# Performance work log

Measured on AMD Instinct MI355X. Metric: run time of the kernel, lower is better.

## Reference

```python
import jax, jax.numpy as jnp
import numpy as np

B, L, C = 4, 2048, 512
H, D = 8, 512          # n_head, hidden_dim (per-head dim)
TEMP = 1.0
EPS = 1e-5


def setup_inputs() -> dict:
    key = jax.random.key(0)
    ks = jax.random.split(key, 12)
    s_in = 1.0 / np.sqrt(C)
    s_out = 1.0 / np.sqrt(H * D)
    return {
        "q": jax.random.normal(ks[0], (B, L, C), jnp.float32),
        "k": jax.random.normal(ks[1], (B, L, C), jnp.float32),
        "v": jax.random.normal(ks[2], (B, L, C), jnp.float32),
        "mask": jax.random.randint(ks[3], (B, L, L), 0, 2).astype(bool),
        "Wq": jax.random.normal(ks[4], (C, H * D), jnp.float32) * s_in,
        "bq": jnp.zeros((H * D,), jnp.float32),
        "Wk": jax.random.normal(ks[5], (C, H * D), jnp.float32) * s_in,
        "bk": jnp.zeros((H * D,), jnp.float32),
        "Wv": jax.random.normal(ks[6], (C, H * D), jnp.float32) * s_in,
        "bv": jnp.zeros((H * D,), jnp.float32),
        "Wo": jax.random.normal(ks[7], (H * D, D), jnp.float32) * s_out,
        "bo": jnp.zeros((D,), jnp.float32),
        "gamma": jnp.ones((D,), jnp.float32),
        "beta": jnp.zeros((D,), jnp.float32),
    }


def reference(q, k, v, mask, Wq, bq, Wk, bk, Wv, bv, Wo, bo, gamma, beta):
    b, ql, _ = q.shape
    residual = q
    qh = (q @ Wq + bq).reshape(b, ql, H, D)           # b,l,h,d
    kh = (k @ Wk + bk).reshape(b, ql, H, D)
    vh = (v @ Wv + bv).reshape(b, ql, H, D)
    # scores in head-major layout to mirror torch permute(2,0,1,3)
    scores = jnp.einsum("bqhd,bkhd->hbqk", qh, kh) / TEMP  # h,b,l,l
    scores = jnp.where(mask[None], -jnp.inf, scores)
    atten = jax.nn.softmax(scores, axis=-1)                 # h,b,l,l
    ctx = jnp.einsum("hbqk,bkhd->bqhd", atten, vh)          # b,l,h,d
    ctx = ctx.reshape(b, ql, H * D)
    out = ctx @ Wo + bo                                     # b,l,D  (dropout in eval mode)
    x = out + residual
    mu = jnp.mean(x, axis=-1, keepdims=True)
    var = jnp.var(x, axis=-1, keepdims=True)
    out = (x - mu) / jnp.sqrt(var + EPS) * gamma + beta
    return out, atten.reshape(H * b, ql, ql)
```

## Files before the change

### kernel.cpp

```cpp
#include <hip/hip_runtime.h>
#include <stdint.h>


typedef unsigned short u16;
typedef _Float16 f16;
typedef __attribute__((ext_vector_type(4))) _Float16 f16x4;
typedef __attribute__((ext_vector_type(8))) _Float16 f16x8;
typedef __attribute__((ext_vector_type(4))) float f32x4;

#define EPI_QKH    0
#define EPI_VHT    1
#define EPI_SCORES 2
#define EPI_CTX    3
#define EPI_OUT    4

__device__ __forceinline__ f32x4 mfma16(f16x8 a, f16x8 b, f32x4 c) {
  return __builtin_amdgcn_mfma_f32_16x16x32_f16(a, b, c, 0, 0, 0);
}

__device__ __forceinline__ void stage_tile_f16(const char* gbase, size_t grow, char* lds, int tid) {
  const int lane = tid & 63, wave = tid >> 6;
#pragma unroll
  for (int c = 0; c < 2; ++c) {
    int chunk = wave * 2 + c;
    int off = chunk * 1024 + lane * 16;
    int r = off >> 6;
    int cb = off & 63;
    const char* g = gbase + (size_t)r * grow + cb;
    __builtin_amdgcn_global_load_lds(
        (__attribute__((address_space(1))) void*)g,
        (__attribute__((address_space(3))) void*)(lds + chunk * 1024),
        16, 0, 0);
  }
}

__device__ __forceinline__ f16x8 load_frag16(const char* lds, int row, int kq) {
  return *(const f16x8*)(lds + ((size_t)row * 32 + kq) * 2);
}

template<int EPI>
__global__ __launch_bounds__(512, 2)
void gemm256_k(const char* __restrict__ A, const char* __restrict__ B,
               int lda, int ldb, int K,
               char* __restrict__ C0, const float* __restrict__ bias) {
  __shared__ alignas(16) char smem[3][32768];

  const int tid = threadIdx.x, lane = tid & 63, wave = tid >> 6;
  const int wm = wave >> 2, wn = wave & 3;

  const int nx = gridDim.x, ny = gridDim.y;
  int id = blockIdx.x + nx * blockIdx.y;
  const int chunk = (nx * ny) >> 3;
  id = (id & 7) * chunk + (id >> 3);
  const int m0 = (id % nx) * 256, n0 = (id / nx) * 256;

  const char* pA = A; const char* pB = B;
  if constexpr (EPI == EPI_SCORES) {
    int z = blockIdx.z, h = z >> 2, b = z & 3;
    size_t e2 = ((size_t)b * 2048 * 4096 + (size_t)h * 512) * 2;
    pA += e2; pB += e2;
  } else if constexpr (EPI == EPI_CTX) {
    int z = blockIdx.z, h = z >> 2, b = z & 3;
    pA += ((size_t)z << 22) * 2;
    pB += ((size_t)(b * 8 + h) * 512 * 2048) * 2;
  }

  f32x4 acc[8][4];
#pragma unroll
  for (int i = 0; i < 8; ++i)
#pragma unroll
    for (int j = 0; j < 4; ++j) acc[i][j] = (f32x4){0.f, 0.f, 0.f, 0.f};

  const size_t rowA = (size_t)lda * 2, rowB = (size_t)ldb * 2;
  const char* gA = pA + (size_t)m0 * rowA;
  const char* gB = pB + (size_t)n0 * rowB;

  const int nk = K >> 5;
  const int kq = (lane >> 4) * 8, l15 = lane & 15, quad = lane >> 4;

  stage_tile_f16(gA, rowA, smem[0], tid);
  stage_tile_f16(gB, rowB, smem[0] + 16384, tid);
  stage_tile_f16(gA + 64, rowA, smem[1], tid);
  stage_tile_f16(gB + 64, rowB, smem[1] + 16384, tid);

  int bc = 0;
  for (int kt = 0; kt < nk; ++kt) {
    if (kt + 1 < nk) { asm volatile("s_waitcnt vmcnt(4)" ::: "memory"); }
    else             { asm volatile("s_waitcnt vmcnt(0)" ::: "memory"); }
    __builtin_amdgcn_sched_barrier(0);
    __builtin_amdgcn_s_barrier();
    __builtin_amdgcn_sched_barrier(0);

    if (kt + 2 < nk) {
      int b2 = bc + 2; if (b2 >= 3) b2 -= 3;
      char* nb = smem[b2];
      stage_tile_f16(gA + (size_t)(kt + 2) * 64, rowA, nb, tid);
      stage_tile_f16(gB + (size_t)(kt + 2) * 64, rowB, nb + 16384, tid);
    }

    char* cur = smem[bc];
    f16x8 af[8], bf[4];
#pragma unroll
    for (int mi = 0; mi < 8; ++mi)
      af[mi] = load_frag16(cur, wm * 128 + mi * 16 + l15, kq);
#pragma unroll
    for (int ni = 0; ni < 4; ++ni)
      bf[ni] = load_frag16(cur + 16384, wn * 64 + ni * 16 + l15, kq);

    __builtin_amdgcn_s_setprio(1);
#pragma unroll
    for (int mi = 0; mi < 8; ++mi)
#pragma unroll
      for (int ni = 0; ni < 4; ++ni)
        acc[mi][ni] = mfma16(af[mi], bf[ni], acc[mi][ni]);
    __builtin_amdgcn_s_setprio(0);

    bc = (bc + 1 == 3) ? 0 : bc + 1;
  }

#pragma unroll
  for (int mi = 0; mi < 8; ++mi)
#pragma unroll
    for (int ni = 0; ni < 4; ++ni)
#pragma unroll
      for (int r = 0; r < 4; ++r) {
        int m = m0 + wm * 128 + mi * 16 + quad * 4 + r;
        int n = n0 + wn * 64 + ni * 16 + l15;
        float v = acc[mi][ni][r];
        if constexpr (EPI == EPI_QKH) {
          v += bias[n];
          ((f16*)C0)[(size_t)m * 4096 + n] = (f16)v;
        } else if constexpr (EPI == EPI_VHT) {
          v += bias[m];
          int hh = m >> 9, d = m & 511, bb = n >> 11, ll = n & 2047;
          ((f16*)C0)[(((size_t)(bb * 8 + hh) * 512 + d) << 11) + ll] = (f16)v;
        } else if constexpr (EPI == EPI_SCORES) {
          int z = blockIdx.z;
          ((float*)C0)[((size_t)z << 22) + ((size_t)m << 11) + n] = v;
        } else if constexpr (EPI == EPI_CTX) {
          int z = blockIdx.z, hh = z >> 2, bb = z & 3;
          ((f16*)C0)[((size_t)(bb * 2048 + m) << 12) + hh * 512 + n] = (f16)v;
        }
      }
}

template<int EPI>
__global__ __launch_bounds__(256, 2)
void gemm_k(const char* __restrict__ A, const char* __restrict__ B,
            int lda, int ldb, int K,
            char* __restrict__ C0,
            const float* __restrict__ bias, const float* __restrict__ resid) {
  __shared__ alignas(16) char smem[3 * 16384];

  const int tid = threadIdx.x, lane = tid & 63, wave = tid >> 6;
  const int wm = wave >> 1, wn = wave & 1;

  const int nx = gridDim.x, ny = gridDim.y;
  int id = blockIdx.x + nx * blockIdx.y;
  const int chunk = (nx * ny) >> 3;
  id = (id & 7) * chunk + (id >> 3);
  const int m0 = (id % nx) * 128, n0 = (id / nx) * 128;

  const char* pA = A; const char* pB = B;
  int kz = 0;
  if constexpr (EPI == EPI_OUT) {
    kz = blockIdx.z;
    pA += (size_t)kz * 2048 * 2;
    pB += (size_t)kz * 2048 * 2;
  }

  f32x4 acc[4][4];
#pragma unroll
  for (int i = 0; i < 4; ++i)
#pragma unroll
    for (int j = 0; j < 4; ++j) acc[i][j] = (f32x4){0.f, 0.f, 0.f, 0.f};

  const size_t rowA = (size_t)lda * 2, rowB = (size_t)ldb * 2;
  const char* gA = pA + (size_t)m0 * rowA;
  const char* gB = pB + (size_t)n0 * rowB;

  const int nk = K >> 5;
  const int kq = (lane >> 4) * 8, l15 = lane & 15, quad = lane >> 4;

  stage_tile_f16(gA, rowA, smem, tid);
  stage_tile_f16(gB, rowB, smem + 8192, tid);
  stage_tile_f16(gA + 64, rowA, smem + 16384, tid);
  stage_tile_f16(gB + 64, rowB, smem + 16384 + 8192, tid);

  int bc = 0;
  for (int kt = 0; kt < nk; ++kt) {
    if (kt + 1 < nk) { asm volatile("s_waitcnt vmcnt(4)" ::: "memory"); }
    else             { asm volatile("s_waitcnt vmcnt(0)" ::: "memory"); }
    __builtin_amdgcn_sched_barrier(0);
    __builtin_amdgcn_s_barrier();
    __builtin_amdgcn_sched_barrier(0);

    if (kt + 2 < nk) {
      int b2 = bc + 2; if (b2 >= 3) b2 -= 3;
      char* nb = smem + b2 * 16384;
      stage_tile_f16(gA + (size_t)(kt + 2) * 64, rowA, nb, tid);
      stage_tile_f16(gB + (size_t)(kt + 2) * 64, rowB, nb + 8192, tid);
    }

    char* cur = smem + bc * 16384;
    f16x8 af[4], bf[4];
#pragma unroll
    for (int mi = 0; mi < 4; ++mi)
      af[mi] = load_frag16(cur, wm * 64 + mi * 16 + l15, kq);
#pragma unroll
    for (int ni = 0; ni < 4; ++ni)
      bf[ni] = load_frag16(cur + 8192, wn * 64 + ni * 16 + l15, kq);

    __builtin_amdgcn_s_setprio(1);
#pragma unroll
    for (int mi = 0; mi < 4; ++mi)
#pragma unroll
      for (int ni = 0; ni < 4; ++ni)
        acc[mi][ni] = mfma16(af[mi], bf[ni], acc[mi][ni]);
    __builtin_amdgcn_s_setprio(0);

    bc = (bc + 1 == 3) ? 0 : bc + 1;
  }

#pragma unroll
  for (int mi = 0; mi < 4; ++mi)
#pragma unroll
    for (int ni = 0; ni < 4; ++ni)
#pragma unroll
      for (int r = 0; r < 4; ++r) {
        int m = m0 + wm * 64 + mi * 16 + quad * 4 + r;
        int n = n0 + wn * 64 + ni * 16 + l15;
        float v = acc[mi][ni][r];
        if constexpr (EPI == EPI_OUT) {
          if (kz == 0) v += bias[n] + resid[((size_t)m << 9) + n];
          ((float*)C0)[(size_t)kz * 8192 * 512 + ((size_t)m << 9) + n] = v;
        }
      }
}

__global__ __launch_bounds__(256)
void transpose_cvt_k(const float* __restrict__ in, f16* __restrict__ T,
                     int R, int Cc) {
  __shared__ f16 tile[32][33];
  const int t = threadIdx.x, tc = t & 31, tr = t >> 5;
  const int bx = blockIdx.x, by = blockIdx.y;
#pragma unroll
  for (int k = 0; k < 4; ++k) {
    int r = by * 32 + tr + k * 8;
    tile[tr + k * 8][tc] = (f16)in[(size_t)r * Cc + bx * 32 + tc];
  }
  __syncthreads();
#pragma unroll
  for (int k = 0; k < 4; ++k) {
    int c = bx * 32 + tr + k * 8;
    T[(size_t)c * R + by * 32 + tc] = tile[tc][tr + k * 8];
  }
}

__global__ __launch_bounds__(256)
void cvt_f16_k(const float* __restrict__ in, f16* __restrict__ out) {
  int i = blockIdx.x * 256 + threadIdx.x;
  float4 v = ((const float4*)in)[i];
  f16x4 h;
  h[0] = (f16)v.x; h[1] = (f16)v.y; h[2] = (f16)v.z; h[3] = (f16)v.w;
  ((f16x4*)out)[i] = h;
}

__global__ __launch_bounds__(256)
void maskprep_k(const int* __restrict__ m32, unsigned char* __restrict__ m8) {
  int i = blockIdx.x * 256 + threadIdx.x;
  int4 v = ((const int4*)m32)[i];
  uchar4 c;
  c.x = (unsigned char)v.x; c.y = (unsigned char)v.y;
  c.z = (unsigned char)v.z; c.w = (unsigned char)v.w;
  ((uchar4*)m8)[i] = c;
}

__global__ __launch_bounds__(256)
void softmax_k(float* __restrict__ att, const unsigned char* __restrict__ m8,
               f16* __restrict__ att16) {
  __shared__ float sm[4];
  int t = threadIdx.x, lane = t & 63, wave = t >> 6;
  size_t r = blockIdx.x;
  int z = (int)(r >> 11), m = (int)(r & 2047), b = z & 3;
  float4* row = (float4*)(att + (r << 11));
  const uchar4* mrow = (const uchar4*)(m8 + (((size_t)b << 22) + ((size_t)m << 11)));
  float4 a = row[t], c = row[t + 256];
  uchar4 ma = mrow[t], mc = mrow[t + 256];
  if (ma.x) a.x = -1e30f; if (ma.y) a.y = -1e30f;
  if (ma.z) a.z = -1e30f; if (ma.w) a.w = -1e30f;
  if (mc.x) c.x = -1e30f; if (mc.y) c.y = -1e30f;
  if (mc.z) c.z = -1e30f; if (mc.w) c.w = -1e30f;
  float mx = fmaxf(fmaxf(fmaxf(a.x, a.y), fmaxf(a.z, a.w)),
                   fmaxf(fmaxf(c.x, c.y), fmaxf(c.z, c.w)));
#pragma unroll
  for (int o = 32; o > 0; o >>= 1) mx = fmaxf(mx, __shfl_xor(mx, o));
  if (lane == 0) sm[wave] = mx;
  __syncthreads();
  mx = fmaxf(fmaxf(sm[0], sm[1]), fmaxf(sm[2], sm[3]));
  a.x = __expf(a.x - mx); a.y = __expf(a.y - mx);
  a.z = __expf(a.z - mx); a.w = __expf(a.w - mx);
  c.x = __expf(c.x - mx); c.y = __expf(c.y - mx);
  c.z = __expf(c.z - mx); c.w = __expf(c.w - mx);
  float s = a.x + a.y + a.z + a.w + c.x + c.y + c.z + c.w;
#pragma unroll
  for (int o = 32; o > 0; o >>= 1) s += __shfl_xor(s, o);
  __syncthreads();
  if (lane == 0) sm[wave] = s;
  __syncthreads();
  s = sm[0] + sm[1] + sm[2] + sm[3];
  float inv = 1.0f / s;
  a.x *= inv; a.y *= inv; a.z *= inv; a.w *= inv;
  c.x *= inv; c.y *= inv; c.z *= inv; c.w *= inv;
  row[t] = a; row[t + 256] = c;
  f16x4* r16 = (f16x4*)(att16 + (r << 11));
  f16x4 ha, hc;
  ha[0] = (f16)a.x; ha[1] = (f16)a.y; ha[2] = (f16)a.z; ha[3] = (f16)a.w;
  hc[0] = (f16)c.x; hc[1] = (f16)c.y; hc[2] = (f16)c.z; hc[3] = (f16)c.w;
  r16[t] = ha; r16[t + 256] = hc;
}

__global__ __launch_bounds__(256)
void ln_k(const float* __restrict__ x0, const float* __restrict__ x1,
          const float* __restrict__ gamma, const float* __restrict__ beta,
          float* __restrict__ out) {
  __shared__ float s1[4], s2[4];
  int t = threadIdx.x, lane = t & 63, wave = t >> 6;
  size_t base = (size_t)blockIdx.x << 9;
  float2 va = ((const float2*)(x0 + base))[t];
  float2 vb = ((const float2*)(x1 + base))[t];
  float2 v; v.x = va.x + vb.x; v.y = va.y + vb.y;
  float s = v.x + v.y;
  float q = v.x * v.x + v.y * v.y;
#pragma unroll
  for (int o = 32; o > 0; o >>= 1) { s += __shfl_xor(s, o); q += __shfl_xor(q, o); }
  if (lane == 0) { s1[wave] = s; s2[wave] = q; }
  __syncthreads();
  s = s1[0] + s1[1] + s1[2] + s1[3];
  q = s2[0] + s2[1] + s2[2] + s2[3];
  float mu = s * (1.0f / 512.0f);
  float var = q * (1.0f / 512.0f) - mu * mu;
  float rs = rsqrtf(var + 1e-5f);
  float2 g = ((const float2*)gamma)[t];
  float2 bb = ((const float2*)beta)[t];
  float2 o2;
  o2.x = (v.x - mu) * rs * g.x + bb.x;
  o2.y = (v.y - mu) * rs * g.y + bb.y;
  ((float2*)(out + base))[t] = o2;
}

extern "C" void kernel_launch(void* const* d_in, const int* in_sizes, int n_in,
                              void* d_out, int out_size, void* d_ws, size_t ws_size,
                              hipStream_t stream) {
  (void)in_sizes; (void)n_in; (void)out_size; (void)ws_size;
  const float* q     = (const float*)d_in[0];
  const float* k     = (const float*)d_in[1];
  const float* v     = (const float*)d_in[2];
  const int*   mask  = (const int*)d_in[3];
  const float* Wq    = (const float*)d_in[4];
  const float* bq    = (const float*)d_in[5];
  const float* Wk    = (const float*)d_in[6];
  const float* bk    = (const float*)d_in[7];
  const float* Wv    = (const float*)d_in[8];
  const float* bv    = (const float*)d_in[9];
  const float* Wo    = (const float*)d_in[10];
  const float* bo    = (const float*)d_in[11];
  const float* gamma = (const float*)d_in[12];
  const float* beta  = (const float*)d_in[13];

  float* out0  = (float*)d_out;
  float* atten = out0 + (size_t)4 * 2048 * 512;

  char* ws = (char*)d_ws;
  const size_t MB = 1024ull * 1024ull;
  f16* WqT  = (f16*)(ws + 0 * MB);
  f16* WkT  = (f16*)(ws + 4 * MB);
  f16* WvT  = (f16*)(ws + 8 * MB);
  f16* WoT  = (f16*)(ws + 12 * MB);
  unsigned char* mask8 = (unsigned char*)(ws + 16 * MB);
  f16* q16  = (f16*)(ws + 32 * MB);
  f16* k16  = (f16*)(ws + 40 * MB);
  f16* v16  = (f16*)(ws + 48 * MB);
  f16* vhT  = (f16*)(ws + 56 * MB);
  f16* atten16 = (f16*)(ws + 120 * MB);
  f16* qh   = (f16*)(ws + 120 * MB);
  f16* kh   = (f16*)(ws + 184 * MB);
  f16* ctx  = (f16*)(ws + 376 * MB);
  float* xbuf = (float*)(ws + 120 * MB);

  transpose_cvt_k<<<dim3(128, 16), 256, 0, stream>>>(Wq, WqT, 512, 4096);
  transpose_cvt_k<<<dim3(128, 16), 256, 0, stream>>>(Wk, WkT, 512, 4096);
  transpose_cvt_k<<<dim3(128, 16), 256, 0, stream>>>(Wv, WvT, 512, 4096);
  transpose_cvt_k<<<dim3(16, 128), 256, 0, stream>>>(Wo, WoT, 4096, 512);
  maskprep_k<<<16384, 256, 0, stream>>>(mask, mask8);
  cvt_f16_k<<<4096, 256, 0, stream>>>(q, q16);
  cvt_f16_k<<<4096, 256, 0, stream>>>(k, k16);
  cvt_f16_k<<<4096, 256, 0, stream>>>(v, v16);

  gemm256_k<EPI_QKH><<<dim3(32, 16, 1), 512, 0, stream>>>(
      (const char*)q16, (const char*)WqT, 512, 512, 512, (char*)qh, bq);
  gemm256_k<EPI_QKH><<<dim3(32, 16, 1), 512, 0, stream>>>(
      (const char*)k16, (const char*)WkT, 512, 512, 512, (char*)kh, bk);

  gemm256_k<EPI_VHT><<<dim3(16, 32, 1), 512, 0, stream>>>(
      (const char*)WvT, (const char*)v16, 512, 512, 512, (char*)vhT, bv);

  gemm256_k<EPI_SCORES><<<dim3(8, 8, 32), 512, 0, stream>>>(
      (const char*)qh, (const char*)kh, 4096, 4096, 512, (char*)atten, nullptr);

  softmax_k<<<65536, 256, 0, stream>>>(atten, mask8, atten16);

  gemm256_k<EPI_CTX><<<dim3(8, 2, 32), 512, 0, stream>>>(
      (const char*)atten16, (const char*)vhT, 2048, 2048, 2048, (char*)ctx, nullptr);

  gemm_k<EPI_OUT><<<dim3(64, 4, 2), 256, 0, stream>>>(
      (const char*)ctx, (const char*)WoT, 4096, 4096, 2048, (char*)xbuf, bo, q);

  ln_k<<<8192, 256, 0, stream>>>(xbuf, xbuf + (size_t)8192 * 512, gamma, beta, out0);
}
```

Before: 1.495 ms.

## Restructure 256-tile GEMM into K=64 double-buffered, XOR-swizzled, four-phase pipeline

Replaces the triple-buffered K=32 tile loop of the 256x256 GEMM with a double-buffered K=64 scheme. Each tile is split into four 128-row halves that are staged one at a time between four MFMA phases, so loads for the next tile overlap compute on the current one. LDS rows are 128 bytes with an XOR swizzle on the column to reduce bank conflicts on fragment reads. The cost is more barriers per iteration and 128KB of LDS per block, which may limit occupancy relative to the previous 96KB.

Result: no change. 1.486 ms (-0.6%).

```diff
diff --git a/kernel.cpp b/kernel.cpp
--- a/kernel.cpp
+++ b/kernel.cpp
@@ -18,40 +18,41 @@
   return __builtin_amdgcn_mfma_f32_16x16x32_f16(a, b, c, 0, 0, 0);
 }
 
-__device__ __forceinline__ void stage_tile_f16(const char* gbase, size_t grow, char* lds, int tid) {
-  const int lane = tid & 63, wave = tid >> 6;
+__device__ __forceinline__ void stage_half(const char* ghalf, size_t grow,
+                                           char* ldshalf, int tid) {
 #pragma unroll
   for (int c = 0; c < 2; ++c) {
-    int chunk = wave * 2 + c;
-    int off = chunk * 1024 + lane * 16;
-    int r = off >> 6;
-    int cb = off & 63;
-    const char* g = gbase + (size_t)r * grow + cb;
+    int d = c * 8192 + tid * 16;
+    int r = d >> 7;
+    int c2l = (d & 127) ^ ((r & 7) << 4);
+    const char* g = ghalf + (size_t)r * grow + c2l;
     __builtin_amdgcn_global_load_lds(
         (__attribute__((address_space(1))) void*)g,
-        (__attribute__((address_space(3))) void*)(lds + chunk * 1024),
+        (__attribute__((address_space(3))) void*)(ldshalf + d),
         16, 0, 0);
   }
 }
 
-__device__ __forceinline__ f16x8 load_frag16(const char* lds, int row, int kq) {
-  return *(const f16x8*)(lds + ((size_t)row * 32 + kq) * 2);
+__device__ __forceinline__ f16x8 frag_swz(const char* ldshalf, int r, int kbyte) {
+  return *(const f16x8*)(ldshalf + r * 128 + (kbyte ^ ((r & 7) << 4)));
 }
 
 template<int EPI>
 __global__ __launch_bounds__(512, 2)
-void gemm256_k(const char* __restrict__ A, const char* __restrict__ B,
-               int lda, int ldb, int K,
-               char* __restrict__ C0, const float* __restrict__ bias) {
-  __shared__ alignas(16) char smem[3][32768];
+void gemm256p_k(const char* __restrict__ A, const char* __restrict__ B,
+                int lda, int ldb, int K,
+                char* __restrict__ C0, const float* __restrict__ bias) {
+  __shared__ alignas(16) char smem[2][65536];
 
   const int tid = threadIdx.x, lane = tid & 63, wave = tid >> 6;
   const int wm = wave >> 2, wn = wave & 3;
+  const int l15 = lane & 15, quad = lane >> 4;
+  const int kb = quad * 16;
 
   const int nx = gridDim.x, ny = gridDim.y;
   int id = blockIdx.x + nx * blockIdx.y;
-  const int chunk = (nx * ny) >> 3;
-  id = (id & 7) * chunk + (id >> 3);
+  const int chunkw = (nx * ny) >> 3;
+  id = (id & 7) * chunkw + (id >> 3);
   const int m0 = (id % nx) * 256, n0 = (id / nx) * 256;
 
   const char* pA = A; const char* pB = B;
@@ -72,50 +73,115 @@
     for (int j = 0; j < 4; ++j) acc[i][j] = (f32x4){0.f, 0.f, 0.f, 0.f};
 
   const size_t rowA = (size_t)lda * 2, rowB = (size_t)ldb * 2;
-  const char* gA = pA + (size_t)m0 * rowA;
-  const char* gB = pB + (size_t)n0 * rowB;
-
-  const int nk = K >> 5;
-  const int kq = (lane >> 4) * 8, l15 = lane & 15, quad = lane >> 4;
-
-  stage_tile_f16(gA, rowA, smem[0], tid);
-  stage_tile_f16(gB, rowB, smem[0] + 16384, tid);
-  stage_tile_f16(gA + 64, rowA, smem[1], tid);
-  stage_tile_f16(gB + 64, rowB, smem[1] + 16384, tid);
-
-  int bc = 0;
-  for (int kt = 0; kt < nk; ++kt) {
-    if (kt + 1 < nk) { asm volatile("s_waitcnt vmcnt(4)" ::: "memory"); }
-    else             { asm volatile("s_waitcnt vmcnt(0)" ::: "memory"); }
+  const char* gA0 = pA + (size_t)m0 * rowA;
+  const char* gA1 = gA0 + (size_t)128 * rowA;
+  const char* gB0 = pB + (size_t)n0 * rowB;
+  const char* gB1 = gB0 + (size_t)128 * rowB;
+
+  const int nt = K >> 6;
+
+  stage_half(gA0, rowA, smem[0],         tid);
+  stage_half(gA1, rowA, smem[0] + 16384, tid);
+  stage_half(gB0, rowB, smem[0] + 32768, tid);
+  stage_half(gB1, rowB, smem[0] + 49152, tid);
+  if (nt > 1) {
+    stage_half(gA0 + 128, rowA, smem[1], tid);
+    asm volatile("s_waitcnt vmcnt(2)" ::: "memory");
+  } else {
+    asm volatile("s_waitcnt vmcnt(0)" ::: "memory");
+  }
+  __builtin_amdgcn_sched_barrier(0);
+  __builtin_amdgcn_s_barrier();
+  __builtin_amdgcn_sched_barrier(0);
+
+  for (int t = 0; t < nt; ++t) {
+    char* cb = smem[t & 1];
+    char* nb = smem[(t + 1) & 1];
+    const char* myA = cb + wm * 16384;
+    const char* myB = cb + 32768 + (wn >> 1) * 16384;
+    const int rb = (wn & 1) * 64;
+    const size_t ko1 = (size_t)(t + 1) * 128;
+    const size_t ko2 = (size_t)(t + 2) * 128;
+
+    f16x8 a[8], b01[4], b23[4];
+
+    if (t + 1 < nt) stage_half(gA1 + ko1, rowA, nb + 16384, tid);
+#pragma unroll
+    for (int mi = 0; mi < 4; ++mi) {
+      a[mi * 2]     = frag_swz(myA, mi * 16 + l15, kb);
+      a[mi * 2 + 1] = frag_swz(myA, mi * 16 + l15, 64 + kb);
+    }
+#pragma unroll
+    for (int ni = 0; ni < 2; ++ni) {
+      b01[ni * 2]     = frag_swz(myB, rb + ni * 16 + l15, kb);
+      b01[ni * 2 + 1] = frag_swz(myB, rb + ni * 16 + l15, 64 + kb);
+    }
+    __builtin_amdgcn_s_setprio(1);
+#pragma unroll
+    for (int mi = 0; mi < 4; ++mi)
+#pragma unroll
+      for (int ni = 0; ni < 2; ++ni) {
+        acc[mi][ni] = mfma16(a[mi * 2],     b01[ni * 2],     acc[mi][ni]);
+        acc[mi][ni] = mfma16(a[mi * 2 + 1], b01[ni * 2 + 1], acc[mi][ni]);
+      }
+    __builtin_amdgcn_s_setprio(0);
     __builtin_amdgcn_sched_barrier(0);
     __builtin_amdgcn_s_barrier();
     __builtin_amdgcn_sched_barrier(0);
 
-    if (kt + 2 < nk) {
-      int b2 = bc + 2; if (b2 >= 3) b2 -= 3;
-      char* nb = smem[b2];
-      stage_tile_f16(gA + (size_t)(kt + 2) * 64, rowA, nb, tid);
-      stage_tile_f16(gB + (size_t)(kt + 2) * 64, rowB, nb + 16384, tid);
+    if (t + 1 < nt) stage_half(gB0 + ko1, rowB, nb + 32768, tid);
+#pragma unroll
+    for (int ni = 0; ni < 2; ++ni) {
+      b23[ni * 2]     = frag_swz(myB, rb + (ni + 2) * 16 + l15, kb);
+      b23[ni * 2 + 1] = frag_swz(myB, rb + (ni + 2) * 16 + l15, 64 + kb);
     }
-
-    char* cur = smem[bc];
-    f16x8 af[8], bf[4];
-#pragma unroll
-    for (int mi = 0; mi < 8; ++mi)
-      af[mi] = load_frag16(cur, wm * 128 + mi * 16 + l15, kq);
-#pragma unroll
-    for (int ni = 0; ni < 4; ++ni)
-      bf[ni] = load_frag16(cur + 16384, wn * 64 + ni * 16 + l15, kq);
-
     __builtin_amdgcn_s_setprio(1);
 #pragma unroll
-    for (int mi = 0; mi < 8; ++mi)
-#pragma unroll
-      for (int ni = 0; ni < 4; ++ni)
-        acc[mi][ni] = mfma16(af[mi], bf[ni], acc[mi][ni]);
+    for (int mi = 0; mi < 4; ++mi)
+#pragma unroll
+      for (int ni = 0; ni < 2; ++ni) {
+        acc[mi][ni + 2] = mfma16(a[mi * 2],     b23[ni * 2],     acc[mi][ni + 2]);
+        acc[mi][ni + 2] = mfma16(a[mi * 2 + 1], b23[ni * 2 + 1], acc[mi][ni + 2]);
+      }
     __builtin_amdgcn_s_setprio(0);
-
-    bc = (bc + 1 == 3) ? 0 : bc + 1;
+    __builtin_amdgcn_sched_barrier(0);
+    __builtin_amdgcn_s_barrier();
+    __builtin_amdgcn_sched_barrier(0);
+
+    if (t + 1 < nt) stage_half(gB1 + ko1, rowB, nb + 49152, tid);
+#pragma unroll
+    for (int mi = 0; mi < 4; ++mi) {
+      a[mi * 2]     = frag_swz(myA, (mi + 4) * 16 + l15, kb);
+      a[mi * 2 + 1] = frag_swz(myA, (mi + 4) * 16 + l15, 64 + kb);
+    }
+    __builtin_amdgcn_s_setprio(1);
+#pragma unroll
+    for (int mi = 0; mi < 4; ++mi)
+#pragma unroll
+      for (int ni = 0; ni < 2; ++ni) {
+        acc[mi + 4][ni + 2] = mfma16(a[mi * 2],     b23[ni * 2],     acc[mi + 4][ni + 2]);
+        acc[mi + 4][ni + 2] = mfma16(a[mi * 2 + 1], b23[ni * 2 + 1], acc[mi + 4][ni + 2]);
+      }
+    __builtin_amdgcn_s_setprio(0);
+    __builtin_amdgcn_sched_barrier(0);
+    __builtin_amdgcn_s_barrier();
+    __builtin_amdgcn_sched_barrier(0);
+
+    if (t + 2 < nt) stage_half(gA0 + ko2, rowA, cb, tid);
+    __builtin_amdgcn_s_setprio(1);
+#pragma unroll
+    for (int mi = 0; mi < 4; ++mi)
+#pragma unroll
+      for (int ni = 0; ni < 2; ++ni) {
+        acc[mi + 4][ni] = mfma16(a[mi * 2],     b01[ni * 2],     acc[mi + 4][ni]);
+        acc[mi + 4][ni] = mfma16(a[mi * 2 + 1], b01[ni * 2 + 1], acc[mi + 4][ni]);
+      }
+    __builtin_amdgcn_s_setprio(0);
+    if (t + 2 < nt) { asm volatile("s_waitcnt vmcnt(2)" ::: "memory"); }
+    else            { asm volatile("s_waitcnt vmcnt(0)" ::: "memory"); }
+    __builtin_amdgcn_sched_barrier(0);
+    __builtin_amdgcn_s_barrier();
+    __builtin_amdgcn_sched_barrier(0);
   }
 
 #pragma unroll
@@ -144,6 +210,26 @@
       }
 }
 
+__device__ __forceinline__ void stage_tile_f16(const char* gbase, size_t grow, char* lds, int tid) {
+  const int lane = tid & 63, wave = tid >> 6;
+#pragma unroll
+  for (int c = 0; c < 2; ++c) {
+    int chunk = wave * 2 + c;
+    int off = chunk * 1024 + lane * 16;
+    int r = off >> 6;
+    int cby = off & 63;
+    const char* g = gbase + (size_t)r * grow + cby;
+    __builtin_amdgcn_global_load_lds(
+        (__attribute__((address_space(1))) void*)g,
+        (__attribute__((address_space(3))) void*)(lds + chunk * 1024),
+        16, 0, 0);
+  }
+}
+
+__device__ __forceinline__ f16x8 load_frag16(const char* lds, int row, int kq) {
+  return *(const f16x8*)(lds + ((size_t)row * 32 + kq) * 2);
+}
+
 template<int EPI>
 __global__ __launch_bounds__(256, 2)
 void gemm_k(const char* __restrict__ A, const char* __restrict__ B,
@@ -397,20 +483,20 @@
   cvt_f16_k<<<4096, 256, 0, stream>>>(k, k16);
   cvt_f16_k<<<4096, 256, 0, stream>>>(v, v16);
 
-  gemm256_k<EPI_QKH><<<dim3(32, 16, 1), 512, 0, stream>>>(
+  gemm256p_k<EPI_QKH><<<dim3(32, 16, 1), 512, 0, stream>>>(
       (const char*)q16, (const char*)WqT, 512, 512, 512, (char*)qh, bq);
-  gemm256_k<EPI_QKH><<<dim3(32, 16, 1), 512, 0, stream>>>(
+  gemm256p_k<EPI_QKH><<<dim3(32, 16, 1), 512, 0, stream>>>(
       (const char*)k16, (const char*)WkT, 512, 512, 512, (char*)kh, bk);
 
-  gemm256_k<EPI_VHT><<<dim3(16, 32, 1), 512, 0, stream>>>(
+  gemm256p_k<EPI_VHT><<<dim3(16, 32, 1), 512, 0, stream>>>(
       (const char*)WvT, (const char*)v16, 512, 512, 512, (char*)vhT, bv);
 
-  gemm256_k<EPI_SCORES><<<dim3(8, 8, 32), 512, 0, stream>>>(
+  gemm256p_k<EPI_SCORES><<<dim3(8, 8, 32), 512, 0, stream>>>(
       (const char*)qh, (const char*)kh, 4096, 4096, 512, (char*)atten, nullptr);
 
   softmax_k<<<65536, 256, 0, stream>>>(atten, mask8, atten16);
 
-  gemm256_k<EPI_CTX><<<dim3(8, 2, 32), 512, 0, stream>>>(
+  gemm256p_k<EPI_CTX><<<dim3(8, 2, 32), 512, 0, stream>>>(
       (const char*)atten16, (const char*)vhT, 2048, 2048, 2048, (char*)ctx, nullptr);
 
   gemm_k<EPI_OUT><<<dim3(64, 4, 2), 256, 0, stream>>>(
```
